# Kernel tuning notes

Hardware: AMD Instinct MI355X
Metric: run time of the kernel (lower is better)

Reference implementation:

```python
import jax, jax.numpy as jnp
import numpy as np

D = 768      # d_model == d_patch (16*16*3)
DFF = 3072
NH = 12
DH = D // NH  # 64
P = 16
IMG = 224
HP = IMG // P  # 14
NP = HP * HP   # 196
L = NP + 1     # 197 with CLS
NL = 12        # layers (weights SHARED across layers, per original code)
NC = 1000


def _pos_enc(length, d):
    # Faithful to PositionalEncoding: even dims sin with exponent i, odd dims cos with exponent i-1
    pos = jnp.arange(length, dtype=jnp.float32)[:, None]          # [L,1]
    dim = jnp.arange(d)
    i = jnp.where(dim % 2 == 0, dim, (dim // 2) * 2).astype(jnp.float32)
    ang = pos / jnp.power(10000.0, i / d)                          # [L,D]
    return jnp.where(dim % 2 == 0, jnp.sin(ang), jnp.cos(ang))


def _ln(x, g, b, eps=1e-5):
    m = x.mean(-1, keepdims=True)
    v = x.var(-1, keepdims=True)
    return (x - m) / jnp.sqrt(v + eps) * g + b


def setup_inputs() -> dict:
    key = jax.random.key(0)
    ks = jax.random.split(key, 12)
    s = 0.02
    n = lambda k, shp: jax.random.normal(k, shp, jnp.float32) * s
    return {
        "x": jax.random.normal(ks[0], (32, 3, IMG, IMG), jnp.float32),
        "w_proj": n(ks[1], (D, D)), "b_proj": jnp.zeros((D,), jnp.float32),
        "cls_emb": jnp.zeros((1, 1, D), jnp.float32),
        "ln1_g": jnp.ones((D,), jnp.float32), "ln1_b": jnp.zeros((D,), jnp.float32),
        "w_qkv": n(ks[2], (3 * D, D)), "b_qkv": jnp.zeros((3 * D,), jnp.float32),
        "w_o": n(ks[3], (D, D)), "b_o": jnp.zeros((D,), jnp.float32),
        "ln2_g": jnp.ones((D,), jnp.float32), "ln2_b": jnp.zeros((D,), jnp.float32),
        "w_fc1": n(ks[4], (DFF, D)), "b_fc1": jnp.zeros((DFF,), jnp.float32),
        "w_fc2": n(ks[5], (D, DFF)), "b_fc2": jnp.zeros((D,), jnp.float32),
        "lnf_g": jnp.ones((D,), jnp.float32), "lnf_b": jnp.zeros((D,), jnp.float32),
        "w_h": n(ks[6], (D, D)), "b_h": jnp.zeros((D,), jnp.float32),
        "w_c": n(ks[7], (NC, D)), "b_c": jnp.zeros((NC,), jnp.float32),
    }


def reference(x, w_proj, b_proj, cls_emb, ln1_g, ln1_b, w_qkv, b_qkv, w_o, b_o,
              ln2_g, ln2_b, w_fc1, b_fc1, w_fc2, b_fc2, lnf_g, lnf_b,
              w_h, b_h, w_c, b_c):
    b = x.shape[0]
    # convert_to_patch: unfold -> channel-major patch features [b, NP, 3*P*P]
    patches = x.reshape(b, 3, HP, P, HP, P).transpose(0, 2, 4, 1, 3, 5).reshape(b, NP, 3 * P * P)
    emb = patches @ w_proj.T + b_proj                              # [b,NP,D]
    cls = jnp.broadcast_to(cls_emb, (b, 1, D))
    h = jnp.concatenate([cls, emb], axis=1) + _pos_enc(L, D)[None]  # [b,L,D]

    inv_sqrt_dk = 1.0 / jnp.sqrt(jnp.float32(DH))
    for _ in range(NL):  # SAME weights every layer (faithful to nn.Sequential of one object)
        y = _ln(h, ln1_g, ln1_b)
        qkv = y @ w_qkv.T + b_qkv                                   # [b,L,3D]
        # faithful non-standard head split: view(b,l,3*DH,NH).transpose -> [b,NH,L,3*DH]
        qkv = qkv.reshape(b, L, 3 * DH, NH).transpose(0, 3, 1, 2)
        q, k, v = jnp.split(qkv, 3, axis=-1)                        # each [b,NH,L,DH]
        attn = jax.nn.softmax(jnp.einsum('bhld,bhmd->bhlm', q, k) * inv_sqrt_dk, axis=-1)
        o = jnp.einsum('bhlm,bhmd->bhld', attn, v)                  # [b,NH,L,DH]
        o = o.transpose(0, 2, 1, 3).reshape(b, L, D)
        h = h + (o @ w_o.T + b_o)
        y = _ln(h, ln2_g, ln2_b)
        f = jax.nn.gelu(y @ w_fc1.T + b_fc1, approximate=False) @ w_fc2.T + b_fc2
        h = h + f

    rep = _ln(h[:, 0], lnf_g, lnf_b)                                # [b,D]
    hid = jnp.tanh(rep @ w_h.T + b_h)                               # is_pretrain=True
    return hid @ w_c.T + b_c                                        # [b,NC]
```

## Files before the change

kernel.cpp:

```cpp
#include <hip/hip_runtime.h>
#include <hip/hip_bf16.h>


typedef __bf16 bf16;
typedef __bf16 bf16x8 __attribute__((ext_vector_type(8)));
typedef __bf16 bf16x4 __attribute__((ext_vector_type(4)));
typedef float  f32x4  __attribute__((ext_vector_type(4)));

typedef __attribute__((address_space(1))) const unsigned int gu32;
typedef __attribute__((address_space(3))) unsigned int lu32;

static __device__ __forceinline__ f32x4 mfma_bf16(bf16x8 a, bf16x8 b, f32x4 c) {
  return __builtin_amdgcn_mfma_f32_16x16x32_bf16(a, b, c, 0, 0, 0);
}
static __device__ __forceinline__ void gll16(const bf16* g, bf16* l) {
  __builtin_amdgcn_global_load_lds((gu32*)g, (lu32*)l, 16, 0, 0);
}


__global__ __launch_bounds__(256) void f2b_k(const float* __restrict__ a, bf16* __restrict__ o, int n) {
  int i = blockIdx.x * 256 + threadIdx.x;
  if (i < n) o[i] = (bf16)a[i];
}

__global__ __launch_bounds__(256) void posenc_k(float* __restrict__ pos) {
  int l = blockIdx.x;
  for (int d = threadIdx.x; d < 768; d += 256) {
    int ieff = d & ~1;
    float ang = (float)l * expf(-(float)ieff * (9.210340371976184f / 768.0f));
    pos[l * 768 + d] = (d & 1) ? cosf(ang) : sinf(ang);
  }
}

__global__ __launch_bounds__(256) void patchify_k(const float* __restrict__ x, bf16* __restrict__ p) {
  int idx = blockIdx.x * 256 + threadIdx.x;
  int t = idx / 768, col = idx - t * 768;
  int b = t / 196, pp = t - b * 196;
  int ph = pp / 14, pw = pp - ph * 14;
  int c = col >> 8, r = col & 255, i = r >> 4, j = r & 15;
  p[idx] = (bf16)x[((b * 3 + c) * 224 + ph * 16 + i) * 224 + pw * 16 + j];
}

__global__ __launch_bounds__(256) void combine_k(float* __restrict__ h, const float* __restrict__ pos,
                                                 const float* __restrict__ cls) {
  int idx = blockIdx.x * 256 + threadIdx.x;
  int t = idx / 768, d = idx - t * 768;
  int l = t % 197;
  float p = pos[l * 768 + d];
  if (l == 0) h[idx] = cls[d] + p;
  else        h[idx] += p;
}

template<int PAD>
__global__ __launch_bounds__(256) void ln4_k(const float* __restrict__ x, const float* __restrict__ g,
                                             const float* __restrict__ bb, bf16* __restrict__ y,
                                             int nrows, int instride) {
  const int wave = threadIdx.x >> 6, lane = threadIdx.x & 63;
  const int row = blockIdx.x * 4 + wave;
  if (row >= nrows) return;
  const float4* x4 = (const float4*)(x + (size_t)row * instride);
  float4 v0 = x4[lane], v1 = x4[lane + 64], v2 = x4[lane + 128];
  float s  = v0.x + v0.y + v0.z + v0.w + v1.x + v1.y + v1.z + v1.w + v2.x + v2.y + v2.z + v2.w;
  float s2 = v0.x*v0.x + v0.y*v0.y + v0.z*v0.z + v0.w*v0.w
           + v1.x*v1.x + v1.y*v1.y + v1.z*v1.z + v1.w*v1.w
           + v2.x*v2.x + v2.y*v2.y + v2.z*v2.z + v2.w*v2.w;
  #pragma unroll
  for (int o = 1; o < 64; o <<= 1) { s += __shfl_xor(s, o); s2 += __shfl_xor(s2, o); }
  float m = s * (1.0f / 768.0f);
  float inv = rsqrtf(s2 * (1.0f / 768.0f) - m * m + 1e-5f);
  int orow = row;
  if (PAD) { int bq = row / 197; orow = row + bq * 3; }
  bf16* yr = y + (size_t)orow * 768;
  const float4* g4 = (const float4*)g;
  const float4* b4 = (const float4*)bb;
  #pragma unroll
  for (int i = 0; i < 3; ++i) {
    int idx = lane + i * 64;
    float4 vv = (i == 0) ? v0 : (i == 1) ? v1 : v2;
    float4 gv = g4[idx], bv = b4[idx];
    bf16x4 o;
    o[0] = (bf16)((vv.x - m) * inv * gv.x + bv.x);
    o[1] = (bf16)((vv.y - m) * inv * gv.y + bv.y);
    o[2] = (bf16)((vv.z - m) * inv * gv.z + bv.z);
    o[3] = (bf16)((vv.w - m) * inv * gv.w + bv.w);
    *(bf16x4*)(yr + idx * 4) = o;
  }
}

template<int BN, int EPI>
__global__ __launch_bounds__(256) void gemm2(
    const bf16* __restrict__ A, const bf16* __restrict__ B,
    int M, int N, int K, int ldc, const float* __restrict__ bias,
    float* __restrict__ outF, bf16* __restrict__ outB)
{
  constexpr int WN = (BN == 128) ? 64 : 32;
  constexpr int NI = WN / 16;
  constexpr int NB = BN / 32;
  __shared__ alignas(16) bf16 As[128 * 64];
  __shared__ alignas(16) bf16 Bs[BN * 64];
  const int tid = threadIdx.x;
  const int lane = tid & 63, wave = tid >> 6;
  const int wr = wave >> 1, wc = wave & 1;
  const int lrow = lane & 15, lgrp = lane >> 4;
  const int row0 = blockIdx.x * 128, col0 = blockIdx.y * BN;

  f32x4 acc[4][NI] = {};
  const bf16* Agb = A + (size_t)row0 * K;
  const bf16* Bgb = B + (size_t)col0 * K;
  const int srow = lane >> 3;
  const int schunk = lane & 7;

  const int nk = K >> 6;
  for (int kt = 0; kt < nk; ++kt) {
    const bf16* Ag = Agb + kt * 64;
    const bf16* Bg = Bgb + kt * 64;
    #pragma unroll
    for (int i = 0; i < 4; ++i) {
      int rr = (wave * 4 + i) * 8 + srow;
      int g = schunk ^ (rr & 7);
      gll16(Ag + (size_t)rr * K + g * 8, As + (wave * 4 + i) * 512);
    }
    #pragma unroll
    for (int i = 0; i < NB; ++i) {
      int rr = (wave * NB + i) * 8 + srow;
      int g = schunk ^ (rr & 7);
      gll16(Bg + (size_t)rr * K + g * 8, Bs + (wave * NB + i) * 512);
    }
    __syncthreads();
    #pragma unroll
    for (int kk = 0; kk < 2; ++kk) {
      bf16x8 af[4], bfr[NI];
      #pragma unroll
      for (int mi = 0; mi < 4; ++mi) {
        int r = wr * 64 + mi * 16 + lrow;
        af[mi] = *(const bf16x8*)(As + r * 64 + (((kk * 4 + lgrp) ^ (r & 7)) << 3));
      }
      #pragma unroll
      for (int ni = 0; ni < NI; ++ni) {
        int r = wc * WN + ni * 16 + lrow;
        bfr[ni] = *(const bf16x8*)(Bs + r * 64 + (((kk * 4 + lgrp) ^ (r & 7)) << 3));
      }
      #pragma unroll
      for (int mi = 0; mi < 4; ++mi)
        #pragma unroll
        for (int ni = 0; ni < NI; ++ni)
          acc[mi][ni] = mfma_bf16(af[mi], bfr[ni], acc[mi][ni]);
    }
    __syncthreads();
  }

  #pragma unroll
  for (int ni = 0; ni < NI; ++ni) {
    const int col = col0 + wc * WN + ni * 16 + lrow;
    float bs = 0.0f;
    if (EPI != 1) {
      if (EPI == 5) bs = (col < N) ? bias[col] : 0.0f;
      else          bs = bias[col];
    }
    #pragma unroll
    for (int mi = 0; mi < 4; ++mi) {
      const int rbase = row0 + wr * 64 + mi * 16 + (lgrp << 2);
      #pragma unroll
      for (int j = 0; j < 4; ++j) {
        const int t = rbase + j;
        if (EPI == 1) {
          float val = acc[mi][ni][j] + bias[t];
          if (t < 768) val *= 0.125f;
          outB[(size_t)t * ldc + col] = (bf16)val;
        } else {
          if (t >= M) continue;
          float val = acc[mi][ni][j] + bs;
          if (EPI == 0) {
            int b = t / 196, p = t - b * 196;
            outF[((size_t)(b * 197 + 1 + p)) * 768 + col] = val;
          } else if (EPI == 2) {
            outF[(size_t)t * 768 + col] += val;
          } else if (EPI == 3) {
            outB[(size_t)t * 3072 + col] = (bf16)(0.5f * val * (1.0f + erff(val * 0.70710678118654752f)));
          } else if (EPI == 4) {
            outB[(size_t)t * 768 + col] = (bf16)tanhf(val);
          } else {
            if (col < N) outF[(size_t)t * ldc + col] = val;
          }
        }
      }
    }
  }
}

__global__ __launch_bounds__(512) void attn_k(const bf16* __restrict__ Ct, bf16* __restrict__ O) {
  __shared__ alignas(16) bf16 Ks[208 * 64];
  __shared__ alignas(16) bf16 Qs[208 * 64];
  __shared__ alignas(16) bf16 Vs[64 * 232];
  __shared__ alignas(16) bf16 Ps[8][16 * 232];
  const int bh = blockIdx.x;
  const int b = bh / 12, hh = bh - b * 12;
  const int tid = threadIdx.x, lane = tid & 63, wave = tid >> 6;
  const int lrow = lane & 15, lgrp = lane >> 4;
  const size_t tc0 = (size_t)b * 200;

  for (int task = tid; task < 1600; task += 512) {
    int d = task / 25, lc = task - d * 25;
    int l0 = lc * 8;
    const size_t cb = tc0 + l0;
    bf16x8 qv = *(const bf16x8*)(Ct + ((size_t)(d * 12 + hh)) * 6400 + cb);
    bf16x8 kv = *(const bf16x8*)(Ct + ((size_t)(768 + d * 12 + hh)) * 6400 + cb);
    bf16x8 vv = *(const bf16x8*)(Ct + ((size_t)(1536 + d * 12 + hh)) * 6400 + cb);
    #pragma unroll
    for (int e = 0; e < 8; ++e) {
      int l = l0 + e;
      int sw = ((((d >> 3) ^ (l & 7)) << 3) | (d & 7));
      Ks[l * 64 + sw] = kv[e];
      Qs[l * 64 + sw] = qv[e];
    }
    *(bf16x8*)(Vs + d * 232 + l0) = vv;
  }
  for (int q = tid; q < 64 * 35; q += 512) {
    int d = q / 35, c = 197 + (q - d * 35);
    Vs[d * 232 + c] = (bf16)0.0f;
  }
  __syncthreads();

  for (int rt = wave; rt < 13; rt += 8) {
    const int r = rt * 16 + lrow;
    bf16x8 a0 = *(const bf16x8*)(Qs + r * 64 + ((lgrp ^ (r & 7)) << 3));
    bf16x8 a1 = *(const bf16x8*)(Qs + r * 64 + (((4 + lgrp) ^ (r & 7)) << 3));
    f32x4 sacc[13];
    #pragma unroll
    for (int ct = 0; ct < 13; ++ct) {
      const int kr = ct * 16 + lrow;
      bf16x8 b0 = *(const bf16x8*)(Ks + kr * 64 + ((lgrp ^ (kr & 7)) << 3));
      bf16x8 b1 = *(const bf16x8*)(Ks + kr * 64 + (((4 + lgrp) ^ (kr & 7)) << 3));
      f32x4 s = {};
      s = mfma_bf16(a0, b0, s);
      s = mfma_bf16(a1, b1, s);
      sacc[ct] = s;
    }
    bf16* Pw = Ps[wave];
    float inv4[4];
    #pragma unroll
    for (int j = 0; j < 4; ++j) {
      const int prow = (lgrp << 2) + j;
      float mx = -3.0e38f;
      #pragma unroll
      for (int ct = 0; ct < 13; ++ct) {
        int c = ct * 16 + lrow;
        if (c < 197) mx = fmaxf(mx, sacc[ct][j]);
      }
      #pragma unroll
      for (int o = 1; o < 16; o <<= 1) mx = fmaxf(mx, __shfl_xor(mx, o));
      float sum = 0.0f;
      #pragma unroll
      for (int ct = 0; ct < 13; ++ct) {
        int c = ct * 16 + lrow;
        float p = (c < 197) ? __expf(sacc[ct][j] - mx) : 0.0f;
        sum += p;
        Pw[prow * 232 + c] = (bf16)p;
      }
      #pragma unroll
      for (int o = 1; o < 16; o <<= 1) sum += __shfl_xor(sum, o);
      inv4[j] = 1.0f / sum;
      Pw[prow * 232 + 208 + lrow] = (bf16)0.0f;
    }
    f32x4 oacc[4] = {};
    #pragma unroll
    for (int mc = 0; mc < 7; ++mc) {
      bf16x8 pa = *(const bf16x8*)(Pw + lrow * 232 + mc * 32 + (lgrp << 3));
      #pragma unroll
      for (int n2 = 0; n2 < 4; ++n2) {
        bf16x8 vb = *(const bf16x8*)(Vs + (n2 * 16 + lrow) * 232 + mc * 32 + (lgrp << 3));
        oacc[n2] = mfma_bf16(pa, vb, oacc[n2]);
      }
    }
    #pragma unroll
    for (int n2 = 0; n2 < 4; ++n2) {
      const int d = n2 * 16 + lrow;
      #pragma unroll
      for (int j = 0; j < 4; ++j) {
        const int qrow = rt * 16 + (lgrp << 2) + j;
        if (qrow < 197)
          O[((size_t)b * 197 + qrow) * 768 + hh * 64 + d] = (bf16)(oacc[n2][j] * inv4[j]);
      }
    }
  }
}


extern "C" void kernel_launch(void* const* d_in, const int* in_sizes, int n_in,
                              void* d_out, int out_size, void* d_ws, size_t ws_size,
                              hipStream_t stream) {
  const float* x      = (const float*)d_in[0];
  const float* w_proj = (const float*)d_in[1];
  const float* b_proj = (const float*)d_in[2];
  const float* cls    = (const float*)d_in[3];
  const float* ln1g   = (const float*)d_in[4];
  const float* ln1b   = (const float*)d_in[5];
  const float* w_qkv  = (const float*)d_in[6];
  const float* b_qkv  = (const float*)d_in[7];
  const float* w_o    = (const float*)d_in[8];
  const float* b_o    = (const float*)d_in[9];
  const float* ln2g   = (const float*)d_in[10];
  const float* ln2b   = (const float*)d_in[11];
  const float* w_fc1  = (const float*)d_in[12];
  const float* b_fc1  = (const float*)d_in[13];
  const float* w_fc2  = (const float*)d_in[14];
  const float* b_fc2  = (const float*)d_in[15];
  const float* lnfg   = (const float*)d_in[16];
  const float* lnfb   = (const float*)d_in[17];
  const float* w_h    = (const float*)d_in[18];
  const float* b_h    = (const float*)d_in[19];
  const float* w_c    = (const float*)d_in[20];
  const float* b_c    = (const float*)d_in[21];
  float* out = (float*)d_out;

  uint8_t* ws = (uint8_t*)d_ws;
  size_t off = 0;
  auto alloc = [&](size_t bytes) -> void* {
    void* p = ws + off; off += (bytes + 255) & ~(size_t)255; return p;
  };
  float* h    = (float*)alloc(6400ull * 768 * 4);
  bf16*  ybf  = (bf16*) alloc(6400ull * 768 * 2);
  bf16*  ct   = (bf16*) alloc(2304ull * 6400 * 2);
  bf16*  ob   = (bf16*) alloc(6400ull * 768 * 2);
  bf16*  f1   = (bf16*) alloc(6400ull * 3072 * 2);
  float* pos  = (float*)alloc(197ull * 768 * 4);
  bf16* wprojB = (bf16*)alloc(768ull * 768 * 2);
  bf16* wqkvB  = (bf16*)alloc(2304ull * 768 * 2);
  bf16* woB    = (bf16*)alloc(768ull * 768 * 2);
  bf16* wfc1B  = (bf16*)alloc(3072ull * 768 * 2);
  bf16* wfc2B  = (bf16*)alloc(768ull * 3072 * 2);
  bf16* whB    = (bf16*)alloc(768ull * 768 * 2);
  bf16* wcB    = (bf16*)alloc(1024ull * 768 * 2);
  bf16* repB   = (bf16*)alloc(128ull * 768 * 2);
  bf16* hidB   = (bf16*)alloc(128ull * 768 * 2);
  bf16* patches = f1;

  f2b_k<<<(768 * 768 + 255) / 256, 256, 0, stream>>>(w_proj, wprojB, 768 * 768);
  f2b_k<<<(2304 * 768 + 255) / 256, 256, 0, stream>>>(w_qkv, wqkvB, 2304 * 768);
  f2b_k<<<(768 * 768 + 255) / 256, 256, 0, stream>>>(w_o, woB, 768 * 768);
  f2b_k<<<(3072 * 768 + 255) / 256, 256, 0, stream>>>(w_fc1, wfc1B, 3072 * 768);
  f2b_k<<<(768 * 3072 + 255) / 256, 256, 0, stream>>>(w_fc2, wfc2B, 768 * 3072);
  f2b_k<<<(768 * 768 + 255) / 256, 256, 0, stream>>>(w_h, whB, 768 * 768);
  f2b_k<<<(1000 * 768 + 255) / 256, 256, 0, stream>>>(w_c, wcB, 1000 * 768);
  posenc_k<<<197, 256, 0, stream>>>(pos);
  patchify_k<<<6272 * 768 / 256, 256, 0, stream>>>(x, patches);
  gemm2<64, 0><<<dim3(49, 12), 256, 0, stream>>>(patches, wprojB, 6272, 768, 768, 768, b_proj, h, nullptr);
  combine_k<<<6304 * 768 / 256, 256, 0, stream>>>(h, pos, cls);

  for (int layer = 0; layer < 12; ++layer) {
    ln4_k<1><<<1576, 256, 0, stream>>>(h, ln1g, ln1b, ybf, 6304, 768);
    gemm2<128, 1><<<dim3(18, 50), 256, 0, stream>>>(wqkvB, ybf, 2304, 6400, 768, 6400, b_qkv, nullptr, ct);
    attn_k<<<384, 512, 0, stream>>>(ct, ob);
    gemm2<64, 2><<<dim3(50, 12), 256, 0, stream>>>(ob, woB, 6304, 768, 768, 768, b_o, h, nullptr);
    ln4_k<0><<<1576, 256, 0, stream>>>(h, ln2g, ln2b, ybf, 6304, 768);
    gemm2<128, 3><<<dim3(50, 24), 256, 0, stream>>>(ybf, wfc1B, 6304, 3072, 768, 3072, b_fc1, nullptr, f1);
    gemm2<64, 2><<<dim3(50, 12), 256, 0, stream>>>(f1, wfc2B, 6304, 768, 3072, 768, b_fc2, h, nullptr);
  }

  ln4_k<0><<<8, 256, 0, stream>>>(h, lnfg, lnfb, repB, 32, 197 * 768);
  gemm2<64, 4><<<dim3(1, 12), 256, 0, stream>>>(repB, whB, 32, 768, 768, 768, b_h, nullptr, hidB);
  gemm2<64, 5><<<dim3(1, 16), 256, 0, stream>>>(hidB, wcB, 32, 1000, 768, 1000, b_c, out, nullptr);
}
```

Measured before the change: 2.756 ms.

## Double-buffer GEMM LDS tiles and add 256x256 tile kernel for QKV/FC1

```diff
diff --git a/kernel.cpp b/kernel.cpp
--- a/kernel.cpp
+++ b/kernel.cpp
@@ -96,8 +96,8 @@
   constexpr int WN = (BN == 128) ? 64 : 32;
   constexpr int NI = WN / 16;
   constexpr int NB = BN / 32;
-  __shared__ alignas(16) bf16 As[128 * 64];
-  __shared__ alignas(16) bf16 Bs[BN * 64];
+  __shared__ alignas(16) bf16 As[2][128 * 64];
+  __shared__ alignas(16) bf16 Bs[2][BN * 64];
   const int tid = threadIdx.x;
   const int lane = tid & 63, wave = tid >> 6;
   const int wr = wave >> 1, wc = wave & 1;
@@ -107,59 +107,183 @@
   f32x4 acc[4][NI] = {};
   const bf16* Agb = A + (size_t)row0 * K;
   const bf16* Bgb = B + (size_t)col0 * K;
-  const int srow = lane >> 3;
-  const int schunk = lane & 7;
-
+  const int srow = lane >> 3, schunk = lane & 7;
   const int nk = K >> 6;
+
+  #pragma unroll
+  for (int i = 0; i < 4; ++i) {
+    int rr = (wave * 4 + i) * 8 + srow;
+    int g = schunk ^ (rr & 7);
+    gll16(Agb + (size_t)rr * K + g * 8, As[0] + (wave * 4 + i) * 512);
+  }
+  #pragma unroll
+  for (int i = 0; i < NB; ++i) {
+    int rr = (wave * NB + i) * 8 + srow;
+    int g = schunk ^ (rr & 7);
+    gll16(Bgb + (size_t)rr * K + g * 8, Bs[0] + (wave * NB + i) * 512);
+  }
+  __syncthreads();
+
+  int cur = 0;
   for (int kt = 0; kt < nk; ++kt) {
-    const bf16* Ag = Agb + kt * 64;
-    const bf16* Bg = Bgb + kt * 64;
-    #pragma unroll
-    for (int i = 0; i < 4; ++i) {
-      int rr = (wave * 4 + i) * 8 + srow;
-      int g = schunk ^ (rr & 7);
-      gll16(Ag + (size_t)rr * K + g * 8, As + (wave * 4 + i) * 512);
-    }
-    #pragma unroll
-    for (int i = 0; i < NB; ++i) {
-      int rr = (wave * NB + i) * 8 + srow;
-      int g = schunk ^ (rr & 7);
-      gll16(Bg + (size_t)rr * K + g * 8, Bs + (wave * NB + i) * 512);
-    }
-    __syncthreads();
+    if (kt + 1 < nk) {
+      const bf16* Ag = Agb + (kt + 1) * 64;
+      const bf16* Bg = Bgb + (kt + 1) * 64;
+      bf16* Ad = As[cur ^ 1]; bf16* Bd = Bs[cur ^ 1];
+      #pragma unroll
+      for (int i = 0; i < 4; ++i) {
+        int rr = (wave * 4 + i) * 8 + srow;
+        int g = schunk ^ (rr & 7);
+        gll16(Ag + (size_t)rr * K + g * 8, Ad + (wave * 4 + i) * 512);
+      }
+      #pragma unroll
+      for (int i = 0; i < NB; ++i) {
+        int rr = (wave * NB + i) * 8 + srow;
+        int g = schunk ^ (rr & 7);
+        gll16(Bg + (size_t)rr * K + g * 8, Bd + (wave * NB + i) * 512);
+      }
+    }
+    const bf16* Ac = As[cur]; const bf16* Bc = Bs[cur];
     #pragma unroll
     for (int kk = 0; kk < 2; ++kk) {
       bf16x8 af[4], bfr[NI];
       #pragma unroll
       for (int mi = 0; mi < 4; ++mi) {
         int r = wr * 64 + mi * 16 + lrow;
-        af[mi] = *(const bf16x8*)(As + r * 64 + (((kk * 4 + lgrp) ^ (r & 7)) << 3));
+        af[mi] = *(const bf16x8*)(Ac + r * 64 + (((kk * 4 + lgrp) ^ (r & 7)) << 3));
       }
       #pragma unroll
       for (int ni = 0; ni < NI; ++ni) {
         int r = wc * WN + ni * 16 + lrow;
-        bfr[ni] = *(const bf16x8*)(Bs + r * 64 + (((kk * 4 + lgrp) ^ (r & 7)) << 3));
-      }
+        bfr[ni] = *(const bf16x8*)(Bc + r * 64 + (((kk * 4 + lgrp) ^ (r & 7)) << 3));
+      }
+      __builtin_amdgcn_s_setprio(1);
       #pragma unroll
       for (int mi = 0; mi < 4; ++mi)
         #pragma unroll
         for (int ni = 0; ni < NI; ++ni)
           acc[mi][ni] = mfma_bf16(af[mi], bfr[ni], acc[mi][ni]);
+      __builtin_amdgcn_s_setprio(0);
     }
     __syncthreads();
+    cur ^= 1;
   }
 
   #pragma unroll
   for (int ni = 0; ni < NI; ++ni) {
     const int col = col0 + wc * WN + ni * 16 + lrow;
-    float bs = 0.0f;
-    if (EPI != 1) {
-      if (EPI == 5) bs = (col < N) ? bias[col] : 0.0f;
-      else          bs = bias[col];
-    }
+    float bs = (EPI == 5) ? ((col < N) ? bias[col] : 0.0f) : bias[col];
     #pragma unroll
     for (int mi = 0; mi < 4; ++mi) {
       const int rbase = row0 + wr * 64 + mi * 16 + (lgrp << 2);
+      #pragma unroll
+      for (int j = 0; j < 4; ++j) {
+        const int t = rbase + j;
+        if (t >= M) continue;
+        float val = acc[mi][ni][j] + bs;
+        if (EPI == 0) {
+          int b = t / 196, p = t - b * 196;
+          outF[((size_t)(b * 197 + 1 + p)) * 768 + col] = val;
+        } else if (EPI == 2) {
+          outF[(size_t)t * 768 + col] += val;
+        } else if (EPI == 4) {
+          outB[(size_t)t * 768 + col] = (bf16)tanhf(val);
+        } else {
+          if (col < N) outF[(size_t)t * ldc + col] = val;
+        }
+      }
+    }
+  }
+}
+
+template<int EPI>
+__global__ __launch_bounds__(512, 2) void gemm3(
+    const bf16* __restrict__ A, const bf16* __restrict__ B,
+    int M, int N, int K, int ldc, const float* __restrict__ bias,
+    bf16* __restrict__ outB)
+{
+  __shared__ alignas(16) bf16 As[2][256 * 64];
+  __shared__ alignas(16) bf16 Bs[2][256 * 64];
+  const int tid = threadIdx.x;
+  const int lane = tid & 63, wave = tid >> 6;
+  const int wm = wave >> 2, wn = wave & 3;
+  const int lrow = lane & 15, lgrp = lane >> 4;
+  const int row0 = blockIdx.x * 256, col0 = blockIdx.y * 256;
+
+  f32x4 acc[8][4] = {};
+  const bf16* Agb = A + (size_t)row0 * K;
+  const bf16* Bgb = B + (size_t)col0 * K;
+  const int srow = lane >> 3, schunk = lane & 7;
+  const int nk = K >> 6;
+
+  #pragma unroll
+  for (int i = 0; i < 4; ++i) {
+    int rr = (wave * 4 + i) * 8 + srow;
+    int g = schunk ^ (rr & 7);
+    gll16(Agb + (size_t)rr * K + g * 8, As[0] + (wave * 4 + i) * 512);
+    gll16(Bgb + (size_t)rr * K + g * 8, Bs[0] + (wave * 4 + i) * 512);
+  }
+  __syncthreads();
+
+  int cur = 0;
+  for (int kt = 0; kt < nk; ++kt) {
+    if (kt + 1 < nk) {
+      const bf16* Ag = Agb + (kt + 1) * 64;
+      const bf16* Bg = Bgb + (kt + 1) * 64;
+      bf16* Ad = As[cur ^ 1]; bf16* Bd = Bs[cur ^ 1];
+      #pragma unroll
+      for (int i = 0; i < 4; ++i) {
+        int rr = (wave * 4 + i) * 8 + srow;
+        int g = schunk ^ (rr & 7);
+        gll16(Ag + (size_t)rr * K + g * 8, Ad + (wave * 4 + i) * 512);
+        gll16(Bg + (size_t)rr * K + g * 8, Bd + (wave * 4 + i) * 512);
+      }
+    }
+    const bf16* Ac = As[cur]; const bf16* Bc = Bs[cur];
+    #pragma unroll
+    for (int kk = 0; kk < 2; ++kk) {
+      bf16x8 af[4], bfr[4];
+      #pragma unroll
+      for (int ni = 0; ni < 4; ++ni) {
+        int r = wn * 64 + ni * 16 + lrow;
+        bfr[ni] = *(const bf16x8*)(Bc + r * 64 + (((kk * 4 + lgrp) ^ (r & 7)) << 3));
+      }
+      #pragma unroll
+      for (int mi = 0; mi < 4; ++mi) {
+        int r = wm * 128 + mi * 16 + lrow;
+        af[mi] = *(const bf16x8*)(Ac + r * 64 + (((kk * 4 + lgrp) ^ (r & 7)) << 3));
+      }
+      __builtin_amdgcn_s_setprio(1);
+      #pragma unroll
+      for (int mi = 0; mi < 4; ++mi)
+        #pragma unroll
+        for (int ni = 0; ni < 4; ++ni)
+          acc[mi][ni] = mfma_bf16(af[mi], bfr[ni], acc[mi][ni]);
+      __builtin_amdgcn_s_setprio(0);
+      #pragma unroll
+      for (int mi = 0; mi < 4; ++mi) {
+        int r = wm * 128 + 64 + mi * 16 + lrow;
+        af[mi] = *(const bf16x8*)(Ac + r * 64 + (((kk * 4 + lgrp) ^ (r & 7)) << 3));
+      }
+      __builtin_amdgcn_s_setprio(1);
+      #pragma unroll
+      for (int mi = 0; mi < 4; ++mi)
+        #pragma unroll
+        for (int ni = 0; ni < 4; ++ni)
+          acc[4 + mi][ni] = mfma_bf16(af[mi], bfr[ni], acc[4 + mi][ni]);
+      __builtin_amdgcn_s_setprio(0);
+    }
+    __syncthreads();
+    cur ^= 1;
+  }
+
+  #pragma unroll
+  for (int ni = 0; ni < 4; ++ni) {
+    const int col = col0 + wn * 64 + ni * 16 + lrow;
+    float bs = (EPI == 3) ? bias[col] : 0.0f;
+    #pragma unroll
+    for (int mi = 0; mi < 8; ++mi) {
+      const int rbase = row0 + wm * 128 + mi * 16 + (lgrp << 2);
       #pragma unroll
       for (int j = 0; j < 4; ++j) {
         const int t = rbase + j;
@@ -170,18 +294,7 @@
         } else {
           if (t >= M) continue;
           float val = acc[mi][ni][j] + bs;
-          if (EPI == 0) {
-            int b = t / 196, p = t - b * 196;
-            outF[((size_t)(b * 197 + 1 + p)) * 768 + col] = val;
-          } else if (EPI == 2) {
-            outF[(size_t)t * 768 + col] += val;
-          } else if (EPI == 3) {
-            outB[(size_t)t * 3072 + col] = (bf16)(0.5f * val * (1.0f + erff(val * 0.70710678118654752f)));
-          } else if (EPI == 4) {
-            outB[(size_t)t * 768 + col] = (bf16)tanhf(val);
-          } else {
-            if (col < N) outF[(size_t)t * ldc + col] = val;
-          }
+          outB[(size_t)t * 3072 + col] = (bf16)(0.5f * val * (1.0f + erff(val * 0.70710678118654752f)));
         }
       }
     }
@@ -349,11 +462,11 @@
 
   for (int layer = 0; layer < 12; ++layer) {
     ln4_k<1><<<1576, 256, 0, stream>>>(h, ln1g, ln1b, ybf, 6304, 768);
-    gemm2<128, 1><<<dim3(18, 50), 256, 0, stream>>>(wqkvB, ybf, 2304, 6400, 768, 6400, b_qkv, nullptr, ct);
+    gemm3<1><<<dim3(9, 25), 512, 0, stream>>>(wqkvB, ybf, 2304, 6400, 768, 6400, b_qkv, ct);
     attn_k<<<384, 512, 0, stream>>>(ct, ob);
     gemm2<64, 2><<<dim3(50, 12), 256, 0, stream>>>(ob, woB, 6304, 768, 768, 768, b_o, h, nullptr);
     ln4_k<0><<<1576, 256, 0, stream>>>(h, ln2g, ln2b, ybf, 6304, 768);
-    gemm2<128, 3><<<dim3(50, 24), 256, 0, stream>>>(ybf, wfc1B, 6304, 3072, 768, 3072, b_fc1, nullptr, f1);
+    gemm3<3><<<dim3(25, 12), 512, 0, stream>>>(ybf, wfc1B, 6304, 3072, 768, 3072, b_fc1, f1);
     gemm2<64, 2><<<dim3(50, 12), 256, 0, stream>>>(f1, wfc2B, 6304, 768, 3072, 768, b_fc2, h, nullptr);
   }
 
```

Result: slower. 3.299 ms (+19.7%).

## Double-buffer GEMM LDS tiles to overlap global loads with MFMA compute

Applied to the files above, without the earlier changes.

```diff
diff --git a/kernel.cpp b/kernel.cpp
--- a/kernel.cpp
+++ b/kernel.cpp
@@ -96,8 +96,8 @@
   constexpr int WN = (BN == 128) ? 64 : 32;
   constexpr int NI = WN / 16;
   constexpr int NB = BN / 32;
-  __shared__ alignas(16) bf16 As[128 * 64];
-  __shared__ alignas(16) bf16 Bs[BN * 64];
+  __shared__ alignas(16) bf16 As[2][128 * 64];
+  __shared__ alignas(16) bf16 Bs[2][BN * 64];
   const int tid = threadIdx.x;
   const int lane = tid & 63, wave = tid >> 6;
   const int wr = wave >> 1, wc = wave & 1;
@@ -107,46 +107,66 @@
   f32x4 acc[4][NI] = {};
   const bf16* Agb = A + (size_t)row0 * K;
   const bf16* Bgb = B + (size_t)col0 * K;
-  const int srow = lane >> 3;
-  const int schunk = lane & 7;
-
+  const int srow = lane >> 3, schunk = lane & 7;
   const int nk = K >> 6;
+
+  #pragma unroll
+  for (int i = 0; i < 4; ++i) {
+    int rr = (wave * 4 + i) * 8 + srow;
+    int g = schunk ^ (rr & 7);
+    gll16(Agb + (size_t)rr * K + g * 8, As[0] + (wave * 4 + i) * 512);
+  }
+  #pragma unroll
+  for (int i = 0; i < NB; ++i) {
+    int rr = (wave * NB + i) * 8 + srow;
+    int g = schunk ^ (rr & 7);
+    gll16(Bgb + (size_t)rr * K + g * 8, Bs[0] + (wave * NB + i) * 512);
+  }
+  __syncthreads();
+
+  int cur = 0;
   for (int kt = 0; kt < nk; ++kt) {
-    const bf16* Ag = Agb + kt * 64;
-    const bf16* Bg = Bgb + kt * 64;
-    #pragma unroll
-    for (int i = 0; i < 4; ++i) {
-      int rr = (wave * 4 + i) * 8 + srow;
-      int g = schunk ^ (rr & 7);
-      gll16(Ag + (size_t)rr * K + g * 8, As + (wave * 4 + i) * 512);
-    }
-    #pragma unroll
-    for (int i = 0; i < NB; ++i) {
-      int rr = (wave * NB + i) * 8 + srow;
-      int g = schunk ^ (rr & 7);
-      gll16(Bg + (size_t)rr * K + g * 8, Bs + (wave * NB + i) * 512);
-    }
-    __syncthreads();
+    if (kt + 1 < nk) {
+      const bf16* Ag = Agb + (kt + 1) * 64;
+      const bf16* Bg = Bgb + (kt + 1) * 64;
+      bf16* Ad = As[cur ^ 1]; bf16* Bd = Bs[cur ^ 1];
+      #pragma unroll
+      for (int i = 0; i < 4; ++i) {
+        int rr = (wave * 4 + i) * 8 + srow;
+        int g = schunk ^ (rr & 7);
+        gll16(Ag + (size_t)rr * K + g * 8, Ad + (wave * 4 + i) * 512);
+      }
+      #pragma unroll
+      for (int i = 0; i < NB; ++i) {
+        int rr = (wave * NB + i) * 8 + srow;
+        int g = schunk ^ (rr & 7);
+        gll16(Bg + (size_t)rr * K + g * 8, Bd + (wave * NB + i) * 512);
+      }
+    }
+    const bf16* Ac = As[cur]; const bf16* Bc = Bs[cur];
     #pragma unroll
     for (int kk = 0; kk < 2; ++kk) {
       bf16x8 af[4], bfr[NI];
       #pragma unroll
       for (int mi = 0; mi < 4; ++mi) {
         int r = wr * 64 + mi * 16 + lrow;
-        af[mi] = *(const bf16x8*)(As + r * 64 + (((kk * 4 + lgrp) ^ (r & 7)) << 3));
+        af[mi] = *(const bf16x8*)(Ac + r * 64 + (((kk * 4 + lgrp) ^ (r & 7)) << 3));
       }
       #pragma unroll
       for (int ni = 0; ni < NI; ++ni) {
         int r = wc * WN + ni * 16 + lrow;
-        bfr[ni] = *(const bf16x8*)(Bs + r * 64 + (((kk * 4 + lgrp) ^ (r & 7)) << 3));
-      }
+        bfr[ni] = *(const bf16x8*)(Bc + r * 64 + (((kk * 4 + lgrp) ^ (r & 7)) << 3));
+      }
+      __builtin_amdgcn_s_setprio(1);
       #pragma unroll
       for (int mi = 0; mi < 4; ++mi)
         #pragma unroll
         for (int ni = 0; ni < NI; ++ni)
           acc[mi][ni] = mfma_bf16(af[mi], bfr[ni], acc[mi][ni]);
+      __builtin_amdgcn_s_setprio(0);
     }
     __syncthreads();
+    cur ^= 1;
   }
 
   #pragma unroll
```

New measurement: 2.962 ms. 1.07x slower.

## Shrink attention LDS footprint, reuse Q buffer for P, fuse posenc into patch GEMM

Applied to the files above, without the earlier changes.

```diff
diff --git a/kernel.cpp b/kernel.cpp
--- a/kernel.cpp
+++ b/kernel.cpp
@@ -41,14 +41,11 @@
   p[idx] = (bf16)x[((b * 3 + c) * 224 + ph * 16 + i) * 224 + pw * 16 + j];
 }
 
-__global__ __launch_bounds__(256) void combine_k(float* __restrict__ h, const float* __restrict__ pos,
-                                                 const float* __restrict__ cls) {
-  int idx = blockIdx.x * 256 + threadIdx.x;
-  int t = idx / 768, d = idx - t * 768;
-  int l = t % 197;
-  float p = pos[l * 768 + d];
-  if (l == 0) h[idx] = cls[d] + p;
-  else        h[idx] += p;
+__global__ __launch_bounds__(256) void cls_k(float* __restrict__ h, const float* __restrict__ pos,
+                                             const float* __restrict__ cls) {
+  int b = blockIdx.x;
+  for (int d = threadIdx.x; d < 768; d += 256)
+    h[((size_t)b * 197) * 768 + d] = cls[d] + pos[d];
 }
 
 template<int PAD>
@@ -91,6 +88,7 @@
 __global__ __launch_bounds__(256) void gemm2(
     const bf16* __restrict__ A, const bf16* __restrict__ B,
     int M, int N, int K, int ldc, const float* __restrict__ bias,
+    const float* __restrict__ posw,
     float* __restrict__ outF, bf16* __restrict__ outB)
 {
   constexpr int WN = (BN == 128) ? 64 : 32;
@@ -107,10 +105,9 @@
   f32x4 acc[4][NI] = {};
   const bf16* Agb = A + (size_t)row0 * K;
   const bf16* Bgb = B + (size_t)col0 * K;
-  const int srow = lane >> 3;
-  const int schunk = lane & 7;
-
+  const int srow = lane >> 3, schunk = lane & 7;
   const int nk = K >> 6;
+
   for (int kt = 0; kt < nk; ++kt) {
     const bf16* Ag = Agb + kt * 64;
     const bf16* Bg = Bgb + kt * 64;
@@ -172,7 +169,7 @@
           float val = acc[mi][ni][j] + bs;
           if (EPI == 0) {
             int b = t / 196, p = t - b * 196;
-            outF[((size_t)(b * 197 + 1 + p)) * 768 + col] = val;
+            outF[((size_t)(b * 197 + 1 + p)) * 768 + col] = val + posw[(size_t)(1 + p) * 768 + col];
           } else if (EPI == 2) {
             outF[(size_t)t * 768 + col] += val;
           } else if (EPI == 3) {
@@ -188,18 +185,18 @@
   }
 }
 
-__global__ __launch_bounds__(512) void attn_k(const bf16* __restrict__ Ct, bf16* __restrict__ O) {
-  __shared__ alignas(16) bf16 Ks[208 * 64];
-  __shared__ alignas(16) bf16 Qs[208 * 64];
-  __shared__ alignas(16) bf16 Vs[64 * 232];
-  __shared__ alignas(16) bf16 Ps[8][16 * 232];
+__global__ __launch_bounds__(256) void attn_k(const bf16* __restrict__ Ct, bf16* __restrict__ O) {
+  __shared__ alignas(16) bf16 smem[40960];
+  bf16* Ks = smem;
+  bf16* QP = smem + 13312;
+  bf16* Vs = smem + 27136;
   const int bh = blockIdx.x;
   const int b = bh / 12, hh = bh - b * 12;
   const int tid = threadIdx.x, lane = tid & 63, wave = tid >> 6;
   const int lrow = lane & 15, lgrp = lane >> 4;
   const size_t tc0 = (size_t)b * 200;
 
-  for (int task = tid; task < 1600; task += 512) {
+  for (int task = tid; task < 1600; task += 256) {
     int d = task / 25, lc = task - d * 25;
     int l0 = lc * 8;
     const size_t cb = tc0 + l0;
@@ -211,20 +208,35 @@
       int l = l0 + e;
       int sw = ((((d >> 3) ^ (l & 7)) << 3) | (d & 7));
       Ks[l * 64 + sw] = kv[e];
-      Qs[l * 64 + sw] = qv[e];
-    }
-    *(bf16x8*)(Vs + d * 232 + l0) = vv;
-  }
-  for (int q = tid; q < 64 * 35; q += 512) {
-    int d = q / 35, c = 197 + (q - d * 35);
-    Vs[d * 232 + c] = (bf16)0.0f;
+      QP[l * 64 + sw] = qv[e];
+    }
+    *(bf16x8*)(Vs + d * 216 + l0) = vv;
+  }
+  for (int t2 = tid; t2 < 64 * 16; t2 += 256) {
+    int d = t2 >> 4, c = 200 + (t2 & 15);
+    Vs[d * 216 + c] = (bf16)0.0f;
   }
   __syncthreads();
 
-  for (int rt = wave; rt < 13; rt += 8) {
-    const int r = rt * 16 + lrow;
-    bf16x8 a0 = *(const bf16x8*)(Qs + r * 64 + ((lgrp ^ (r & 7)) << 3));
-    bf16x8 a1 = *(const bf16x8*)(Qs + r * 64 + (((4 + lgrp) ^ (r & 7)) << 3));
+  bf16x8 qa0[4], qa1[4];
+  #pragma unroll
+  for (int ii = 0; ii < 4; ++ii) {
+    int rt = wave + ii * 4;
+    if (rt < 13) {
+      int r = rt * 16 + lrow;
+      qa0[ii] = *(const bf16x8*)(QP + r * 64 + ((lgrp ^ (r & 7)) << 3));
+      qa1[ii] = *(const bf16x8*)(QP + r * 64 + (((4 + lgrp) ^ (r & 7)) << 3));
+    }
+  }
+  __syncthreads();
+
+  bf16* Pw = QP + wave * (16 * 216);
+  const bf16x8 zv = {};
+
+  #pragma unroll
+  for (int ii = 0; ii < 4; ++ii) {
+    const int rt = wave + ii * 4;
+    if (rt >= 13) break;
     f32x4 sacc[13];
     #pragma unroll
     for (int ct = 0; ct < 13; ++ct) {
@@ -232,11 +244,10 @@
       bf16x8 b0 = *(const bf16x8*)(Ks + kr * 64 + ((lgrp ^ (kr & 7)) << 3));
       bf16x8 b1 = *(const bf16x8*)(Ks + kr * 64 + (((4 + lgrp) ^ (kr & 7)) << 3));
       f32x4 s = {};
-      s = mfma_bf16(a0, b0, s);
-      s = mfma_bf16(a1, b1, s);
+      s = mfma_bf16(qa0[ii], b0, s);
+      s = mfma_bf16(qa1[ii], b1, s);
       sacc[ct] = s;
     }
-    bf16* Pw = Ps[wave];
     float inv4[4];
     #pragma unroll
     for (int j = 0; j < 4; ++j) {
@@ -255,20 +266,28 @@
         int c = ct * 16 + lrow;
         float p = (c < 197) ? __expf(sacc[ct][j] - mx) : 0.0f;
         sum += p;
-        Pw[prow * 232 + c] = (bf16)p;
+        Pw[prow * 216 + c] = (bf16)p;
       }
       #pragma unroll
       for (int o = 1; o < 16; o <<= 1) sum += __shfl_xor(sum, o);
       inv4[j] = 1.0f / sum;
-      Pw[prow * 232 + 208 + lrow] = (bf16)0.0f;
     }
     f32x4 oacc[4] = {};
     #pragma unroll
     for (int mc = 0; mc < 7; ++mc) {
-      bf16x8 pa = *(const bf16x8*)(Pw + lrow * 232 + mc * 32 + (lgrp << 3));
+      bf16x8 pa;
+      if (mc < 6) {
+        pa = *(const bf16x8*)(Pw + lrow * 216 + mc * 32 + (lgrp << 3));
+      } else {
+        pa = *(const bf16x8*)(Pw + lrow * 216 + 192 + ((lgrp & 1) << 3));
+        if (lgrp >= 2) pa = zv;
+      }
       #pragma unroll
       for (int n2 = 0; n2 < 4; ++n2) {
-        bf16x8 vb = *(const bf16x8*)(Vs + (n2 * 16 + lrow) * 232 + mc * 32 + (lgrp << 3));
+        const int vr = n2 * 16 + lrow;
+        bf16x8 vb;
+        if (mc < 6) vb = *(const bf16x8*)(Vs + vr * 216 + mc * 32 + (lgrp << 3));
+        else        vb = *(const bf16x8*)(Vs + vr * 216 + 192 + ((lgrp & 1) << 3));
         oacc[n2] = mfma_bf16(pa, vb, oacc[n2]);
       }
     }
@@ -344,20 +363,27 @@
   f2b_k<<<(1000 * 768 + 255) / 256, 256, 0, stream>>>(w_c, wcB, 1000 * 768);
   posenc_k<<<197, 256, 0, stream>>>(pos);
   patchify_k<<<6272 * 768 / 256, 256, 0, stream>>>(x, patches);
-  gemm2<64, 0><<<dim3(49, 12), 256, 0, stream>>>(patches, wprojB, 6272, 768, 768, 768, b_proj, h, nullptr);
-  combine_k<<<6304 * 768 / 256, 256, 0, stream>>>(h, pos, cls);
+  gemm2<64, 0><<<dim3(49, 12), 256, 0, stream>>>(patches, wprojB, 6272, 768, 768, 768,
+                                                 b_proj, pos, h, nullptr);
+  cls_k<<<32, 256, 0, stream>>>(h, pos, cls);
 
   for (int layer = 0; layer < 12; ++layer) {
     ln4_k<1><<<1576, 256, 0, stream>>>(h, ln1g, ln1b, ybf, 6304, 768);
-    gemm2<128, 1><<<dim3(18, 50), 256, 0, stream>>>(wqkvB, ybf, 2304, 6400, 768, 6400, b_qkv, nullptr, ct);
-    attn_k<<<384, 512, 0, stream>>>(ct, ob);
-    gemm2<64, 2><<<dim3(50, 12), 256, 0, stream>>>(ob, woB, 6304, 768, 768, 768, b_o, h, nullptr);
+    gemm2<128, 1><<<dim3(18, 50), 256, 0, stream>>>(wqkvB, ybf, 2304, 6400, 768, 6400,
+                                                    b_qkv, nullptr, nullptr, ct);
+    attn_k<<<384, 256, 0, stream>>>(ct, ob);
+    gemm2<64, 2><<<dim3(50, 12), 256, 0, stream>>>(ob, woB, 6304, 768, 768, 768,
+                                                   b_o, nullptr, h, nullptr);
     ln4_k<0><<<1576, 256, 0, stream>>>(h, ln2g, ln2b, ybf, 6304, 768);
-    gemm2<128, 3><<<dim3(50, 24), 256, 0, stream>>>(ybf, wfc1B, 6304, 3072, 768, 3072, b_fc1, nullptr, f1);
-    gemm2<64, 2><<<dim3(50, 12), 256, 0, stream>>>(f1, wfc2B, 6304, 768, 3072, 768, b_fc2, h, nullptr);
+    gemm2<128, 3><<<dim3(50, 24), 256, 0, stream>>>(ybf, wfc1B, 6304, 3072, 768, 3072,
+                                                    b_fc1, nullptr, nullptr, f1);
+    gemm2<64, 2><<<dim3(50, 12), 256, 0, stream>>>(f1, wfc2B, 6304, 768, 3072, 768,
+                                                   b_fc2, nullptr, h, nullptr);
   }
 
   ln4_k<0><<<8, 256, 0, stream>>>(h, lnfg, lnfb, repB, 32, 197 * 768);
-  gemm2<64, 4><<<dim3(1, 12), 256, 0, stream>>>(repB, whB, 32, 768, 768, 768, b_h, nullptr, hidB);
-  gemm2<64, 5><<<dim3(1, 16), 256, 0, stream>>>(hidB, wcB, 32, 1000, 768, 1000, b_c, out, nullptr);
-}
+  gemm2<64, 4><<<dim3(1, 12), 256, 0, stream>>>(repB, whB, 32, 768, 768, 768,
+                                                b_h, nullptr, nullptr, hidB);
+  gemm2<64, 5><<<dim3(1, 16), 256, 0, stream>>>(hidB, wcB, 32, 1000, 768, 1000,
+                                                b_c, nullptr, out, nullptr);
+}
```

After: 2.761 ms. About the same (+0.2%).
